# Kernel tuning notes

Hardware: AMD Instinct MI355X
Metric: run time of the kernel (lower is better)

Reference implementation:

```python
import jax, jax.numpy as jnp
import numpy as np

N_HEADS = 16
EPSILON = 0.01
SCORE_SCALE = 1.0
C_CONST = 2.0 + EPSILON


def setup_inputs() -> dict:
    key = jax.random.key(0)
    k1, k2, k3 = jax.random.split(key, 3)
    B, T, D = 2, 2048, 1024
    x = jax.random.normal(k1, (B, T, D), dtype=jnp.float32)
    # torch nn.Linear convention: weight [out_features, in_features], y = x @ W.T
    Wqkv = jax.random.normal(k2, (3 * D, D), dtype=jnp.float32) * (1.0 / np.sqrt(D))
    Wout = jax.random.normal(k3, (D, D), dtype=jnp.float32) * (1.0 / np.sqrt(D))
    return {"x": x, "Wqkv": Wqkv, "Wout": Wout}


def reference(x, Wqkv, Wout):
    B, T, D = x.shape
    H = N_HEADS
    hd = D // H
    qkv = x @ Wqkv.T  # [B, T, 3D]
    q, k, v = jnp.split(qkv, 3, axis=-1)
    # [B, H, T, hd]
    q = q.reshape(B, T, H, hd).transpose(0, 2, 1, 3).astype(jnp.float32)
    k = k.reshape(B, T, H, hd).transpose(0, 2, 1, 3).astype(jnp.float32)
    v = v.reshape(B, T, H, hd).transpose(0, 2, 1, 3).astype(jnp.float32)
    # L2 normalize along head dim (F.normalize uses eps=1e-12 via clamp of norm)
    qn = q / jnp.maximum(jnp.linalg.norm(q, axis=-1, keepdims=True), 1e-12)
    kn = k / jnp.maximum(jnp.linalg.norm(k, axis=-1, keepdims=True), 1e-12)
    # full T x T kernel matrix per (batch, head)
    x_dot = jnp.einsum("bhtd,bhsd->bhts", qn, kn)
    denom = jnp.maximum(C_CONST - 2.0 * x_dot, 1e-6)
    K = (x_dot * x_dot) / denom * SCORE_SCALE
    causal = jnp.tril(jnp.ones((T, T), dtype=bool))  # keep lower triangle incl. diag
    K = jnp.where(causal[None, None, :, :], K, 0.0)
    numerator = jnp.einsum("bhts,bhsd->bhtd", K, v)
    denominator = jnp.sum(K, axis=-1, keepdims=True)
    out = numerator / (denominator + 1e-6)
    out = out.transpose(0, 2, 1, 3).reshape(B, T, D)
    return out @ Wout.T
```

## Files before the change

### kernel.cpp

```cpp
#include <hip/hip_runtime.h>
#include <hip/hip_bf16.h>

#define T_SEQ 2048
#define D_MODEL 1024
#define BT 4096
#define QKV_N 3072

typedef __attribute__((ext_vector_type(8))) short bf16x8;
typedef __attribute__((ext_vector_type(4))) short bf16x4;
typedef __attribute__((ext_vector_type(4))) float f32x4;

typedef unsigned int __attribute__((address_space(1))) as1_uint;
typedef unsigned int __attribute__((address_space(3))) as3_uint;

__device__ __forceinline__ unsigned short f2bf(float f) {
    unsigned u = __builtin_bit_cast(unsigned, f);
    u += 0x7fffu + ((u >> 16) & 1u);
    return (unsigned short)(u >> 16);
}
__device__ __forceinline__ float bf2f(unsigned short h) {
    unsigned u = ((unsigned)h) << 16;
    return __builtin_bit_cast(float, u);
}
__device__ __forceinline__ void gload_lds16(const void* g, void* l) {
    __builtin_amdgcn_global_load_lds((const as1_uint*)g, (as3_uint*)l, 16, 0, 0);
}
__device__ __forceinline__ unsigned cvtpk_bf16(float lo, float hi) {
    unsigned r;
    asm("v_cvt_pk_bf16_f32 %0, %1, %2" : "=v"(r) : "v"(lo), "v"(hi));
    return r;
}

__global__ __launch_bounds__(256) void cvt_bf16_3(const float* __restrict__ s0, unsigned short* __restrict__ d0, int n0,
                                                  const float* __restrict__ s1, unsigned short* __restrict__ d1, int n1,
                                                  const float* __restrict__ s2, unsigned short* __restrict__ d2, int n2) {
    int i = blockIdx.x * 256 + threadIdx.x;
    const float* s; unsigned short* d;
    if (i < n0) { s = s0; d = d0; }
    else if (i < n0 + n1) { i -= n0; s = s1; d = d1; }
    else if (i < n0 + n1 + n2) { i -= n0 + n1; s = s2; d = d2; }
    else return;
    const float4* sp = (const float4*)s + (size_t)i * 2;
    const float4 a = sp[0], b = sp[1];
    uint4 o;
    o.x = (unsigned)f2bf(a.x) | ((unsigned)f2bf(a.y) << 16);
    o.y = (unsigned)f2bf(a.z) | ((unsigned)f2bf(a.w) << 16);
    o.z = (unsigned)f2bf(b.x) | ((unsigned)f2bf(b.y) << 16);
    o.w = (unsigned)f2bf(b.z) | ((unsigned)f2bf(b.w) << 16);
    ((uint4*)d)[i] = o;
}

template<int MODE>
__global__ __launch_bounds__(256) void gemm_bt_mfma(const unsigned short* __restrict__ A,
                                                    const unsigned short* __restrict__ B,
                                                    void* __restrict__ Cout,
                                                    unsigned short* __restrict__ qbp,
                                                    unsigned short* __restrict__ kbp,
                                                    int M, int N, int K) {
    __shared__ unsigned short As[128 * 64];
    __shared__ unsigned short Bs[128 * 64];
    const int tid = threadIdx.x;
    const int w = tid >> 6;
    const int l = tid & 63;
    const int l15 = l & 15, l4 = l >> 4;

    const int nblocks = (M / 128) * (N / 128);
    const int cpx = nblocks >> 3;
    const int id2 = (blockIdx.x & 7) * cpx + (blockIdx.x >> 3);
    const int bm = (id2 & 31) * 128;
    const int bn = (id2 >> 5) * 128;

    const int wm = (w >> 1) * 64, wn = (w & 1) * 64;

    const f32x4 z = {0.f, 0.f, 0.f, 0.f};
    f32x4 acc[4][4];
#pragma unroll
    for (int m = 0; m < 4; ++m)
#pragma unroll
        for (int n = 0; n < 4; ++n) acc[m][n] = z;

    const int lrow = l >> 3;
    const int lslot = (l & 7) ^ (lrow & 7);

    for (int k0 = 0; k0 < K; k0 += 64) {
#pragma unroll
        for (int i = 0; i < 4; ++i) {
            const int row = w * 32 + i * 8 + lrow;
            gload_lds16(A + (size_t)(bm + row) * K + k0 + lslot * 8, As + (w * 4 + i) * 512);
            gload_lds16(B + (size_t)(bn + row) * K + k0 + lslot * 8, Bs + (w * 4 + i) * 512);
        }
        __syncthreads();
        bf16x8 af[4][2], bfr[4][2];
#pragma unroll
        for (int m = 0; m < 4; ++m) {
            const int row = wm + m * 16 + l15;
            af[m][0] = *(const bf16x8*)(As + row * 64 + ((l4 ^ (row & 7)) * 8));
            af[m][1] = *(const bf16x8*)(As + row * 64 + (((4 + l4) ^ (row & 7)) * 8));
        }
#pragma unroll
        for (int n = 0; n < 4; ++n) {
            const int row = wn + n * 16 + l15;
            bfr[n][0] = *(const bf16x8*)(Bs + row * 64 + ((l4 ^ (row & 7)) * 8));
            bfr[n][1] = *(const bf16x8*)(Bs + row * 64 + (((4 + l4) ^ (row & 7)) * 8));
        }
#pragma unroll
        for (int m = 0; m < 4; ++m)
#pragma unroll
            for (int n = 0; n < 4; ++n) {
                acc[m][n] = __builtin_amdgcn_mfma_f32_16x16x32_bf16(af[m][0], bfr[n][0], acc[m][n], 0, 0, 0);
                acc[m][n] = __builtin_amdgcn_mfma_f32_16x16x32_bf16(af[m][1], bfr[n][1], acc[m][n], 0, 0, 0);
            }
        __syncthreads();
    }

    if (MODE == 0) {
#pragma unroll
        for (int m = 0; m < 4; ++m)
#pragma unroll
            for (int n = 0; n < 4; ++n)
#pragma unroll
                for (int r = 0; r < 4; ++r) {
                    const int row = bm + wm + m * 16 + l4 * 4 + r;
                    const int col = bn + wn + n * 16 + l15;
                    ((float*)Cout)[(size_t)row * N + col] = acc[m][n][r];
                }
    } else {
        const int gcol0 = bn + wn;
        const int part = gcol0 >> 10;
        const int h = (gcol0 >> 6) & 15;
        if (part < 2) {
            unsigned short* dst = part ? kbp : qbp;
#pragma unroll
            for (int m = 0; m < 4; ++m)
#pragma unroll
                for (int r = 0; r < 4; ++r) {
                    float ss = 0.f;
#pragma unroll
                    for (int n = 0; n < 4; ++n) ss = fmaf(acc[m][n][r], acc[m][n][r], ss);
                    ss += __shfl_xor(ss, 1);
                    ss += __shfl_xor(ss, 2);
                    ss += __shfl_xor(ss, 4);
                    ss += __shfl_xor(ss, 8);
                    const float sc = 1.0f / fmaxf(sqrtf(ss), 1e-12f);
                    const int row = bm + wm + m * 16 + l4 * 4 + r;
                    const int bh2 = (row >> 11) * 16 + h;
                    unsigned short* pdst = dst + ((size_t)bh2 * T_SEQ + (row & 2047)) * 64 + l15;
#pragma unroll
                    for (int n = 0; n < 4; ++n) pdst[n * 16] = f2bf(acc[m][n][r] * sc);
                }
        } else {
            unsigned short* vrow = (unsigned short*)Cout;
            const int vcol0 = gcol0 - 2048;
#pragma unroll
            for (int m = 0; m < 4; ++m)
#pragma unroll
                for (int n = 0; n < 4; ++n)
#pragma unroll
                    for (int r = 0; r < 4; ++r) {
                        const int row = bm + wm + m * 16 + l4 * 4 + r;
                        vrow[(size_t)row * D_MODEL + vcol0 + n * 16 + l15] = f2bf(acc[m][n][r]);
                    }
        }
    }
}

__global__ __launch_bounds__(256) void v_cvt_T(const unsigned short* __restrict__ vrow,
                                               unsigned short* __restrict__ vbT) {
    __shared__ unsigned short tile[64][72];
    const int bh = blockIdx.y;
    const int b = bh >> 4, h = bh & 15;
    const int t0 = blockIdx.x * 64;
    const int r = threadIdx.x >> 2;
    const int c = (threadIdx.x & 3) * 16;
    const unsigned short* src = vrow + (size_t)(b * T_SEQ + t0 + r) * D_MODEL + h * 64 + c;
    uint4 v0 = *(const uint4*)(src);
    uint4 v1 = *(const uint4*)(src + 8);
    unsigned short tmp[16];
    *(uint4*)tmp = v0;
    *(uint4*)(tmp + 8) = v1;
#pragma unroll
    for (int j = 0; j < 16; ++j) tile[c + j][r] = tmp[j];
    __syncthreads();
    const int d = threadIdx.x >> 2;
    const int tc = (threadIdx.x & 3) * 16;
    unsigned short tmp2[16];
#pragma unroll
    for (int j = 0; j < 16; ++j) tmp2[j] = tile[d][tc + j];
    unsigned short* dst = vbT + ((size_t)bh * 64 + d) * T_SEQ + t0 + tc;
    *(uint4*)dst = *(uint4*)tmp2;
    *(uint4*)(dst + 8) = *(uint4*)(tmp2 + 8);
}

#define AT_TS 64

__global__ __launch_bounds__(256, 4) void attn_mfma(const unsigned short* __restrict__ qb,
                                                    const unsigned short* __restrict__ kb,
                                                    const unsigned short* __restrict__ vbT,
                                                    unsigned short* __restrict__ attnb) {
    __shared__ unsigned short Ks[2][64 * 64];
    __shared__ unsigned short Vs[2][64 * 64];

    const int tid = threadIdx.x;
    const int w = tid >> 6;
    const int l = tid & 63;
    const int l15 = l & 15, l4 = l >> 4;

    const int id = blockIdx.x;
    const int xcd = id & 7;
    const int within = id >> 3;
    const int bh = xcd * 4 + (within & 3);
    const int t0i = 31 - (within >> 2);
    const int t0 = t0i * 64;

    const size_t hb = (size_t)bh * T_SEQ * 64;

    const int lrow = l >> 3;
    const int lslot = (l & 7) ^ (lrow & 7);
    const unsigned short* kgp[2];
    const unsigned short* vgp[2];
    unsigned short* kdst[2];
    unsigned short* vdst[2];
#pragma unroll
    for (int c = 0; c < 2; ++c) {
        const int row = w * 16 + c * 8 + lrow;
        kgp[c] = kb + hb + (size_t)row * 64 + lslot * 8;
        vgp[c] = vbT + hb + (size_t)row * T_SEQ + lslot * 8;
        kdst[c] = &Ks[0][(w * 2 + c) * 512];
        vdst[c] = &Vs[0][(w * 2 + c) * 512];
    }

    const int p = l15 & 7;
    const unsigned short* kfp0 = &Ks[0][0] + l15 * 64 + ((l4 ^ p) * 8);
    const unsigned short* kfp1 = &Ks[0][0] + l15 * 64 + (((4 + l4) ^ p) * 8);
    const unsigned short* vfp0 = &Vs[0][0] + l15 * 64 + ((((l4 >> 1) + 0) ^ p) * 8) + (l4 & 1) * 4;
    const unsigned short* vfp1 = &Vs[0][0] + l15 * 64 + ((((l4 >> 1) + 2) ^ p) * 8) + (l4 & 1) * 4;
    const unsigned short* vfp2 = &Vs[0][0] + l15 * 64 + ((((l4 >> 1) + 4) ^ p) * 8) + (l4 & 1) * 4;
    const unsigned short* vfp3 = &Vs[0][0] + l15 * 64 + ((((l4 >> 1) + 6) ^ p) * 8) + (l4 & 1) * 4;

    bf16x8 qf0, qf1;
    {
        const unsigned short* qp = qb + hb + (size_t)(t0 + w * 16 + l15) * 64 + l4 * 8;
        qf0 = *(const bf16x8*)(qp);
        qf1 = *(const bf16x8*)(qp + 32);
    }

    const f32x4 z = {0.f, 0.f, 0.f, 0.f};
    f32x4 acc[4];
#pragma unroll
    for (int i = 0; i < 4; ++i) acc[i] = z;
    float accd = 0.f;

    const int wrow0 = t0 + w * 16;
    const int tq = wrow0 + l15;

#pragma unroll
    for (int c = 0; c < 2; ++c) {
        gload_lds16(kgp[c], kdst[c]);
        gload_lds16(vgp[c], vdst[c]);
    }

    auto compute_tile = [&](int roff, int s0, bool mask) {
        const unsigned short* kc0 = kfp0 + roff;
        const unsigned short* kc1 = kfp1 + roff;
        f32x4 sC[4];
        __builtin_amdgcn_s_setprio(1);
#pragma unroll
        for (int sf = 0; sf < 4; ++sf) {
            bf16x8 kf0 = *(const bf16x8*)(kc0 + sf * 1024);
            bf16x8 kf1 = *(const bf16x8*)(kc1 + sf * 1024);
            f32x4 c = z;
            c = __builtin_amdgcn_mfma_f32_16x16x32_bf16(kf0, qf0, c, 0, 0, 0);
            c = __builtin_amdgcn_mfma_f32_16x16x32_bf16(kf1, qf1, c, 0, 0, 0);
            sC[sf] = c;
        }
        __builtin_amdgcn_s_setprio(0);
        float part_ = 0.f;
#pragma unroll
        for (int sf = 0; sf < 4; ++sf)
#pragma unroll
            for (int r = 0; r < 4; ++r) {
                const float xd = sC[sf][r];
                const float den = __builtin_fmaf(-2.0f, xd, 2.01f);
                float Kv = xd * xd * __builtin_amdgcn_rcpf(den);
                if (mask) {
                    const int s = s0 + sf * 16 + l4 * 4 + r;
                    if (s > tq) Kv = 0.f;
                }
                part_ += Kv;
                sC[sf][r] = Kv;
            }
        accd += part_;
        uint4 p0, p1;
        p0.x = cvtpk_bf16(sC[0][0], sC[0][1]);
        p0.y = cvtpk_bf16(sC[0][2], sC[0][3]);
        p0.z = cvtpk_bf16(sC[1][0], sC[1][1]);
        p0.w = cvtpk_bf16(sC[1][2], sC[1][3]);
        p1.x = cvtpk_bf16(sC[2][0], sC[2][1]);
        p1.y = cvtpk_bf16(sC[2][2], sC[2][3]);
        p1.z = cvtpk_bf16(sC[3][0], sC[3][1]);
        p1.w = cvtpk_bf16(sC[3][2], sC[3][3]);
        const bf16x8 a0 = __builtin_bit_cast(bf16x8, p0);
        const bf16x8 a1 = __builtin_bit_cast(bf16x8, p1);
        const unsigned short* vc0 = vfp0 + roff;
        const unsigned short* vc1 = vfp1 + roff;
        const unsigned short* vc2 = vfp2 + roff;
        const unsigned short* vc3 = vfp3 + roff;
        __builtin_amdgcn_s_setprio(1);
#pragma unroll
        for (int df = 0; df < 4; ++df) {
            const uint2 u0 = *(const uint2*)(vc0 + df * 1024);
            const uint2 u1 = *(const uint2*)(vc1 + df * 1024);
            const uint2 u2 = *(const uint2*)(vc2 + df * 1024);
            const uint2 u3 = *(const uint2*)(vc3 + df * 1024);
            uint4 b0v, b1v;
            b0v.x = u0.x; b0v.y = u0.y; b0v.z = u1.x; b0v.w = u1.y;
            b1v.x = u2.x; b1v.y = u2.y; b1v.z = u3.x; b1v.w = u3.y;
            const bf16x8 B0 = __builtin_bit_cast(bf16x8, b0v);
            const bf16x8 B1 = __builtin_bit_cast(bf16x8, b1v);
            acc[df] = __builtin_amdgcn_mfma_f32_16x16x32_bf16(a0, B0, acc[df], 0, 0, 0);
            acc[df] = __builtin_amdgcn_mfma_f32_16x16x32_bf16(a1, B1, acc[df], 0, 0, 0);
        }
        __builtin_amdgcn_s_setprio(0);
    };

    for (int st = 0; st < t0i; ++st) {
        const int dsto = ((st & 1) ^ 1) * 4096;
#pragma unroll
        for (int c = 0; c < 2; ++c) {
            kgp[c] += 4096;
            vgp[c] += 64;
            gload_lds16(kgp[c], kdst[c] + dsto);
            gload_lds16(vgp[c], vdst[c] + dsto);
        }
        asm volatile("s_waitcnt vmcnt(4)" ::: "memory");
        __builtin_amdgcn_sched_barrier(0);
        __builtin_amdgcn_s_barrier();
        compute_tile((st & 1) * 4096, st * AT_TS, false);
        __builtin_amdgcn_sched_barrier(0);
        __builtin_amdgcn_s_barrier();
    }
    {
        asm volatile("s_waitcnt vmcnt(0)" ::: "memory");
        __builtin_amdgcn_sched_barrier(0);
        __builtin_amdgcn_s_barrier();
        compute_tile((t0i & 1) * 4096, t0i * AT_TS, true);
    }

    accd += __shfl_xor(accd, 16);
    accd += __shfl_xor(accd, 32);

    const int b = bh >> 4, h = bh & 15;
#pragma unroll
    for (int r = 0; r < 4; ++r) {
        const float den = __shfl(accd, l4 * 4 + r) + 1e-6f;
#pragma unroll
        for (int df = 0; df < 4; ++df) {
            const int t = wrow0 + l4 * 4 + r;
            const float o = acc[df][r] / den;
            attnb[((size_t)b * T_SEQ + t) * D_MODEL + h * 64 + df * 16 + l15] = f2bf(o);
        }
    }
}

extern "C" void kernel_launch(void* const* d_in, const int* in_sizes, int n_in,
                              void* d_out, int out_size, void* d_ws, size_t ws_size,
                              hipStream_t stream) {
    const float* x    = (const float*)d_in[0];
    const float* Wqkv = (const float*)d_in[1];
    const float* Wout = (const float*)d_in[2];
    float* out = (float*)d_out;

    char* ws = (char*)d_ws;
    unsigned short* xb    = (unsigned short*)(ws);
    unsigned short* wqkvb = (unsigned short*)(ws + (size_t)8 * 1024 * 1024);
    unsigned short* vrow  = (unsigned short*)(ws + (size_t)16 * 1024 * 1024);
    unsigned short* vbT   = (unsigned short*)(ws + (size_t)24 * 1024 * 1024);
    unsigned short* woutb = (unsigned short*)(ws + (size_t)32 * 1024 * 1024);
    unsigned short* qbp   = (unsigned short*)(ws + (size_t)34 * 1024 * 1024);
    unsigned short* kbp   = (unsigned short*)(ws + (size_t)42 * 1024 * 1024);
    unsigned short* attnb = (unsigned short*)(ws + (size_t)50 * 1024 * 1024);

    cvt_bf16_3<<<4096, 256, 0, stream>>>(x, xb, BT * D_MODEL / 8,
                                         Wqkv, wqkvb, QKV_N * D_MODEL / 8,
                                         Wout, woutb, D_MODEL * D_MODEL / 8);

    gemm_bt_mfma<2><<<(QKV_N / 128) * (BT / 128), 256, 0, stream>>>(
        xb, wqkvb, vrow, qbp, kbp, BT, QKV_N, D_MODEL);

    v_cvt_T<<<dim3(T_SEQ / 64, 32), 256, 0, stream>>>(vrow, vbT);

    attn_mfma<<<1024, 256, 0, stream>>>(qbp, kbp, vbT, attnb);

    gemm_bt_mfma<0><<<(D_MODEL / 128) * (BT / 128), 256, 0, stream>>>(
        attnb, woutb, out, nullptr, nullptr, BT, D_MODEL, D_MODEL);
}
```

Baseline: 176.1 us.

## Pre-permute V transpose layout for 128-bit LDS reads and rebalance causal tile schedule

The V-transpose kernel now writes each row in a permuted 4-element-chunk order. The attention kernel can then copy V tiles unswizzled into LDS and read each MFMA B operand as one 128-bit load instead of four 64-bit loads. The block-to-(head, tile) mapping is also reworked so each XCD pairs heavy and light causal query tiles, replacing the longest-first order. This cuts LDS read instructions in the inner loop. It risks bank conflicts because V rows are no longer XOR-swizzled per row in LDS, and the new scheduling order may change load balance.

```diff
diff --git a/kernel.cpp b/kernel.cpp
--- a/kernel.cpp
+++ b/kernel.cpp
@@ -183,12 +183,17 @@
     __syncthreads();
     const int d = threadIdx.x >> 2;
     const int tc = (threadIdx.x & 3) * 16;
-    unsigned short tmp2[16];
-#pragma unroll
-    for (int j = 0; j < 16; ++j) tmp2[j] = tile[d][tc + j];
-    unsigned short* dst = vbT + ((size_t)bh * 64 + d) * T_SEQ + t0 + tc;
-    *(uint4*)dst = *(uint4*)tmp2;
-    *(uint4*)(dst + 8) = *(uint4*)(tmp2 + 8);
+    const int t5 = tc >> 5, t4 = (tc >> 4) & 1;
+    unsigned short* dstrow = vbT + ((size_t)bh * 64 + d) * T_SEQ + t0;
+    const int dp = d & 7;
+#pragma unroll
+    for (int q = 0; q < 4; ++q) {
+        unsigned short tmp2[4];
+#pragma unroll
+        for (int i = 0; i < 4; ++i) tmp2[i] = tile[d][tc + q * 4 + i];
+        const int slot = (t5 * 4 + q) ^ dp;
+        *(uint2*)(dstrow + slot * 8 + t4 * 4) = *(uint2*)tmp2;
+    }
 }
 
 #define AT_TS 64
@@ -208,8 +213,13 @@
     const int id = blockIdx.x;
     const int xcd = id & 7;
     const int within = id >> 3;
-    const int bh = xcd * 4 + (within & 3);
-    const int t0i = 31 - (within >> 2);
+    const int hl = (((within >> 5) & 1) << 1) | (within & 1);
+    const int vv = (((within >> 6) & 1) << 4) | (((within >> 4) & 1) << 3) |
+                   (((within >> 3) & 1) << 2) | (((within >> 2) & 1) << 1) |
+                   ((within >> 1) & 1);
+    const int pfl = ((within >> 5) & 1) ^ (within & 1);
+    const int bh = xcd * 4 + hl;
+    const int t0i = pfl ? 31 - vv : vv;
     const int t0 = t0i * 64;
 
     const size_t hb = (size_t)bh * T_SEQ * 64;
@@ -224,7 +234,7 @@
     for (int c = 0; c < 2; ++c) {
         const int row = w * 16 + c * 8 + lrow;
         kgp[c] = kb + hb + (size_t)row * 64 + lslot * 8;
-        vgp[c] = vbT + hb + (size_t)row * T_SEQ + lslot * 8;
+        vgp[c] = vbT + hb + (size_t)row * T_SEQ + (l & 7) * 8;
         kdst[c] = &Ks[0][(w * 2 + c) * 512];
         vdst[c] = &Vs[0][(w * 2 + c) * 512];
     }
@@ -232,10 +242,8 @@
     const int p = l15 & 7;
     const unsigned short* kfp0 = &Ks[0][0] + l15 * 64 + ((l4 ^ p) * 8);
     const unsigned short* kfp1 = &Ks[0][0] + l15 * 64 + (((4 + l4) ^ p) * 8);
-    const unsigned short* vfp0 = &Vs[0][0] + l15 * 64 + ((((l4 >> 1) + 0) ^ p) * 8) + (l4 & 1) * 4;
-    const unsigned short* vfp1 = &Vs[0][0] + l15 * 64 + ((((l4 >> 1) + 2) ^ p) * 8) + (l4 & 1) * 4;
-    const unsigned short* vfp2 = &Vs[0][0] + l15 * 64 + ((((l4 >> 1) + 4) ^ p) * 8) + (l4 & 1) * 4;
-    const unsigned short* vfp3 = &Vs[0][0] + l15 * 64 + ((((l4 >> 1) + 6) ^ p) * 8) + (l4 & 1) * 4;
+    const unsigned short* vfp0 = &Vs[0][0] + l15 * 64 + ((l4 ^ p) * 8);
+    const unsigned short* vfp1 = &Vs[0][0] + l15 * 64 + (((4 + l4) ^ p) * 8);
 
     bf16x8 qf0, qf1;
     {
@@ -303,20 +311,11 @@
         const bf16x8 a1 = __builtin_bit_cast(bf16x8, p1);
         const unsigned short* vc0 = vfp0 + roff;
         const unsigned short* vc1 = vfp1 + roff;
-        const unsigned short* vc2 = vfp2 + roff;
-        const unsigned short* vc3 = vfp3 + roff;
         __builtin_amdgcn_s_setprio(1);
 #pragma unroll
         for (int df = 0; df < 4; ++df) {
-            const uint2 u0 = *(const uint2*)(vc0 + df * 1024);
-            const uint2 u1 = *(const uint2*)(vc1 + df * 1024);
-            const uint2 u2 = *(const uint2*)(vc2 + df * 1024);
-            const uint2 u3 = *(const uint2*)(vc3 + df * 1024);
-            uint4 b0v, b1v;
-            b0v.x = u0.x; b0v.y = u0.y; b0v.z = u1.x; b0v.w = u1.y;
-            b1v.x = u2.x; b1v.y = u2.y; b1v.z = u3.x; b1v.w = u3.y;
-            const bf16x8 B0 = __builtin_bit_cast(bf16x8, b0v);
-            const bf16x8 B1 = __builtin_bit_cast(bf16x8, b1v);
+            const bf16x8 B0 = *(const bf16x8*)(vc0 + df * 1024);
+            const bf16x8 B1 = *(const bf16x8*)(vc1 + df * 1024);
             acc[df] = __builtin_amdgcn_mfma_f32_16x16x32_bf16(a0, B0, acc[df], 0, 0, 0);
             acc[df] = __builtin_amdgcn_mfma_f32_16x16x32_bf16(a1, B1, acc[df], 0, 0, 0);
         }
```

Measured after the change: 179.3 us. About the same (+1.8%).
